# Performance work log

Measured on AMD Instinct MI355X. Metric: run time of the kernel, lower is better.

Reference implementation:

```python
import jax, jax.numpy as jnp
import numpy as np

N_NODES = 100000
N_EDGES = 1000000
D_IN = 256
D_OUT = 64


def setup_inputs() -> dict:
    key = jax.random.key(0)
    k1, k2, k3, k4, k5, k6 = jax.random.split(key, 6)
    x = jax.random.normal(k1, (N_NODES, D_IN), dtype=jnp.float32)
    # Xavier-style uniform init: stdv = 1/sqrt(output_dim)
    stdv = 1.0 / np.sqrt(D_OUT)
    weight = jax.random.uniform(k2, (D_IN, D_OUT), dtype=jnp.float32, minval=-stdv, maxval=stdv)
    adj_vals = jax.random.uniform(k3, (N_EDGES,), dtype=jnp.float32)
    prelu_a = jnp.full((1,), 0.25, dtype=jnp.float32)  # nn.PReLU default
    row = jax.random.randint(k4, (N_EDGES,), 0, N_NODES, dtype=jnp.int32)
    col = jax.random.randint(k5, (N_EDGES,), 0, N_NODES, dtype=jnp.int32)
    return {"x": x, "weight": weight, "adj_vals": adj_vals, "prelu_a": prelu_a,
            "row": row, "col": col}


def reference(x, weight, adj_vals, prelu_a, row, col):
    # dense GEMM: [N, D_in] @ [D_in, D_out]
    hidden = x @ weight  # gc_drop=0 -> identity dropout
    # sparse adj spmm: out[i] = sum_{e: row[e]=i} adj_vals[e] * hidden[col[e]]
    msg = adj_vals[:, None] * hidden[col]  # [E, D_out]
    agg = jax.ops.segment_sum(msg, row, num_segments=N_NODES)  # [N, D_out]
    # PReLU with single shared slope
    out = jnp.where(agg > 0, agg, prelu_a * agg)
    return out
```

## Files before the change

### kernel.cpp

```cpp
#include <hip/hip_runtime.h>

#define N_NODES 100000
#define N_EDGES 1000000
#define D_IN    256
#define D_OUT   64

#define BKT_SHIFT   8
#define NODES_PER_B 256
#define N_BKT       391
#define BKT_CAP     3072
#define EPB         8192
#define BIN_BLOCKS  123
#define GEMM_BLOCKS 782
#define NUM_TILES   6250

typedef __attribute__((ext_vector_type(8))) short short8;
typedef __attribute__((ext_vector_type(4))) float f32x4;

__device__ __forceinline__ unsigned short f2bf(float f) {
    unsigned int u = __float_as_uint(f);
    u = (u + 0x7fffu + ((u >> 16) & 1u)) >> 16;
    return (unsigned short)u;
}

__device__ __forceinline__ void mfma_store_tile(
    const short8 afrag[8], const unsigned short wT[64][272],
    unsigned short* __restrict__ hiddenBf, int r0, int n16, int quad)
{
    f32x4 acc[4] = {{0.f,0.f,0.f,0.f},{0.f,0.f,0.f,0.f},
                    {0.f,0.f,0.f,0.f},{0.f,0.f,0.f,0.f}};
#pragma unroll
    for (int ct = 0; ct < 4; ++ct) {
#pragma unroll
        for (int kk = 0; kk < 8; ++kk) {
            short8 b = *(const short8*)&wT[ct * 16 + n16][kk * 32 + quad * 8];
            acc[ct] = __builtin_amdgcn_mfma_f32_16x16x32_bf16(
                afrag[kk], b, acc[ct], 0, 0, 0);
        }
    }
#pragma unroll
    for (int ct = 0; ct < 4; ++ct)
#pragma unroll
        for (int reg = 0; reg < 4; ++reg)
            hiddenBf[(size_t)(r0 + quad * 4 + reg) * D_OUT + ct * 16 + n16]
                = f2bf(acc[ct][reg]);
}

__global__ __launch_bounds__(256, 2) void gemm_bin_kernel(
    const float* __restrict__ x, const float* __restrict__ w,
    unsigned short* __restrict__ hiddenBf,
    const int* __restrict__ row, const int* __restrict__ col,
    const float* __restrict__ adj, int* __restrict__ gCursor,
    int2* __restrict__ edges)
{
    const int t = threadIdx.x;

    if (blockIdx.x < BIN_BLOCKS) {
        __shared__ int cnt[N_BKT];
        __shared__ int cbase[N_BKT];
        __shared__ int cur[N_BKT];

        const int e0 = blockIdx.x * EPB;

        for (int i = t; i < N_BKT; i += 256) cnt[i] = 0;
        __syncthreads();

        for (int i = t; i < EPB; i += 256) {
            int e = e0 + i;
            if (e < N_EDGES) atomicAdd(&cnt[row[e] >> BKT_SHIFT], 1);
        }
        __syncthreads();

        for (int i = t; i < N_BKT; i += 256) {
            int c = cnt[i];
            cbase[i] = c ? atomicAdd(&gCursor[i], c) : 0;
            cur[i] = 0;
        }
        __syncthreads();

        for (int i = t; i < EPB; i += 256) {
            int e = e0 + i;
            if (e < N_EDGES) {
                int r = row[e];
                int b = r >> BKT_SHIFT;
                int off = cbase[b] + atomicAdd(&cur[b], 1);
                if (off < BKT_CAP) {
                    edges[b * BKT_CAP + off] =
                        make_int2(((r & (NODES_PER_B - 1)) << 17) | col[e],
                                  __float_as_int(adj[e]));
                }
            }
        }
        return;
    }

    __shared__ unsigned short wT[64][272];

    for (int i = 0; i < 64; ++i) {
        int idx = t + i * 256;
        int k = idx >> 6, n = idx & 63;
        wT[n][k] = f2bf(w[idx]);
    }
    __syncthreads();

    const int lane = t & 63;
    const int wid  = t >> 6;
    const int n16  = lane & 15;
    const int quad = lane >> 4;

    const int waveGid = (blockIdx.x - BIN_BLOCKS) * 4 + wid;
    const int t0 = waveGid * 2;
    if (t0 >= NUM_TILES) return;

    float4 lo[8], hi[8];
    short8 afrag[8];

    {
        const float* xrow = x + (size_t)(t0 * 16 + n16) * D_IN + quad * 8;
#pragma unroll
        for (int kk = 0; kk < 8; ++kk) {
            lo[kk] = *(const float4*)(xrow + kk * 32);
            hi[kk] = *(const float4*)(xrow + kk * 32 + 4);
        }
    }
#pragma unroll
    for (int kk = 0; kk < 8; ++kk) {
        short8 a;
        a[0] = (short)f2bf(lo[kk].x); a[1] = (short)f2bf(lo[kk].y);
        a[2] = (short)f2bf(lo[kk].z); a[3] = (short)f2bf(lo[kk].w);
        a[4] = (short)f2bf(hi[kk].x); a[5] = (short)f2bf(hi[kk].y);
        a[6] = (short)f2bf(hi[kk].z); a[7] = (short)f2bf(hi[kk].w);
        afrag[kk] = a;
    }

    const int t1 = t0 + 1;
    const bool have1 = t1 < NUM_TILES;
    if (have1) {
        const float* xrow = x + (size_t)(t1 * 16 + n16) * D_IN + quad * 8;
#pragma unroll
        for (int kk = 0; kk < 8; ++kk) {
            lo[kk] = *(const float4*)(xrow + kk * 32);
            hi[kk] = *(const float4*)(xrow + kk * 32 + 4);
        }
    }

    mfma_store_tile(afrag, wT, hiddenBf, t0 * 16, n16, quad);

    if (have1) {
#pragma unroll
        for (int kk = 0; kk < 8; ++kk) {
            short8 a;
            a[0] = (short)f2bf(lo[kk].x); a[1] = (short)f2bf(lo[kk].y);
            a[2] = (short)f2bf(lo[kk].z); a[3] = (short)f2bf(lo[kk].w);
            a[4] = (short)f2bf(hi[kk].x); a[5] = (short)f2bf(hi[kk].y);
            a[6] = (short)f2bf(hi[kk].z); a[7] = (short)f2bf(hi[kk].w);
            afrag[kk] = a;
        }
        mfma_store_tile(afrag, wT, hiddenBf, t1 * 16, n16, quad);
    }
}

__global__ __launch_bounds__(512) void csr_kernel(
    const int2* __restrict__ edges, const int* __restrict__ gCursor,
    int2* __restrict__ csr, unsigned int* __restrict__ startdeg)
{
    __shared__ int cnt[NODES_PER_B];
    __shared__ int cur[NODES_PER_B];

    const int b = blockIdx.x, t = threadIdx.x;
    if (t < NODES_PER_B) cnt[t] = 0;
    __syncthreads();

    const int base = b * BKT_CAP;
    int size = gCursor[b];
    if (size > BKT_CAP) size = BKT_CAP;

    for (int i = t; i < size; i += 512)
        atomicAdd(&cnt[(unsigned)edges[base + i].x >> 17], 1);
    __syncthreads();

    int v = (t < NODES_PER_B) ? cnt[t] : 0;
    for (int off = 1; off < NODES_PER_B; off <<= 1) {
        int tmp = (t < NODES_PER_B && t >= off) ? cnt[t - off] : 0;
        __syncthreads();
        if (t < NODES_PER_B) cnt[t] += tmp;
        __syncthreads();
    }
    if (t < NODES_PER_B) {
        int gstart = base + cnt[t] - v;
        cur[t] = gstart;
        int node = b * NODES_PER_B + t;
        if (node < N_NODES)
            startdeg[node] = ((unsigned)gstart << 11) |
                             (unsigned)(v < 2047 ? v : 2047);
    }
    __syncthreads();

    for (int i = t; i < size; i += 512) {
        int2 rec = edges[base + i];
        int rl = (unsigned)rec.x >> 17;
        int pos = atomicAdd(&cur[rl], 1);
        csr[pos] = make_int2(rec.x & 0x1FFFF, rec.y);
    }
}

__global__ __launch_bounds__(256) void agg_kernel(
    const unsigned short* __restrict__ hiddenBf,
    const unsigned int* __restrict__ startdeg,
    const int2* __restrict__ csr, const float* __restrict__ prelu_a,
    float* __restrict__ out)
{
    const int wid  = threadIdx.x >> 6;
    const int lane = threadIdx.x & 63;
    const int node = blockIdx.x * 4 + wid;

    const unsigned int sd = startdeg[node];
    const int start = sd >> 11;
    const int deg   = sd & 2047;

    float acc = 0.f;
    for (int base = 0; base < deg; base += 64) {
        int take = deg - base;
        if (take > 64) take = 64;
        int2 rec = make_int2(0, 0);
        if (lane < take) rec = csr[start + base + lane];

        int j = 0;
        for (; j + 8 <= take; j += 8) {
            int   c[8]; float v[8]; float h[8];
#pragma unroll
            for (int u = 0; u < 8; ++u) {
                c[u] = __builtin_amdgcn_readlane(rec.x, j + u);
                v[u] = __int_as_float(__builtin_amdgcn_readlane(rec.y, j + u));
            }
#pragma unroll
            for (int u = 0; u < 8; ++u)
                h[u] = __uint_as_float(
                    (unsigned)hiddenBf[(size_t)c[u] * D_OUT + lane] << 16);
#pragma unroll
            for (int u = 0; u < 8; ++u) acc += v[u] * h[u];
        }
        for (; j < take; ++j) {
            int   c = __builtin_amdgcn_readlane(rec.x, j);
            float v = __int_as_float(__builtin_amdgcn_readlane(rec.y, j));
            float h = __uint_as_float(
                (unsigned)hiddenBf[(size_t)c * D_OUT + lane] << 16);
            acc += v * h;
        }
    }
    const float a = prelu_a[0];
    out[(size_t)node * D_OUT + lane] = acc > 0.f ? acc : a * acc;
}

extern "C" void kernel_launch(void* const* d_in, const int* in_sizes, int n_in,
                              void* d_out, int out_size, void* d_ws, size_t ws_size,
                              hipStream_t stream)
{
    const float* x       = (const float*)d_in[0];
    const float* w       = (const float*)d_in[1];
    const float* adj     = (const float*)d_in[2];
    const float* prelu_a = (const float*)d_in[3];
    const int*   row     = (const int*)d_in[4];
    const int*   col     = (const int*)d_in[5];
    float* out = (float*)d_out;

    char* ws = (char*)d_ws;
    unsigned short* hiddenBf = (unsigned short*)(ws);
    int2*  edges    = (int2*)        (ws + 12800000);
    int2*  csr      = (int2*)        (ws + 22409216);
    unsigned int* startdeg = (unsigned int*)(ws + 32018944);
    int*   gCursor  = (int*)         (ws + 32419328);

    hipMemsetAsync(gCursor, 0, N_BKT * sizeof(int), stream);

    gemm_bin_kernel<<<BIN_BLOCKS + GEMM_BLOCKS, 256, 0, stream>>>(
        x, w, hiddenBf, row, col, adj, gCursor, edges);

    csr_kernel<<<N_BKT, 512, 0, stream>>>(edges, gCursor, csr, startdeg);

    agg_kernel<<<N_NODES / 4, 256, 0, stream>>>(hiddenBf, startdeg, csr, prelu_a, out);
}
```

Baseline: 253.8 us.

## Fuse CSR construction and aggregation into one per-bucket kernel with LDS sort

```diff
diff --git a/kernel.cpp b/kernel.cpp
--- a/kernel.cpp
+++ b/kernel.cpp
@@ -22,9 +22,12 @@
     u = (u + 0x7fffu + ((u >> 16) & 1u)) >> 16;
     return (unsigned short)u;
 }
+__device__ __forceinline__ float bf2f(unsigned short h) {
+    return __uint_as_float((unsigned)h << 16);
+}
 
 __device__ __forceinline__ void mfma_store_tile(
-    const short8 afrag[8], const unsigned short wT[64][272],
+    const short8 afrag[8], const unsigned short wT[64][264],
     unsigned short* __restrict__ hiddenBf, int r0, int n16, int quad)
 {
     f32x4 acc[4] = {{0.f,0.f,0.f,0.f},{0.f,0.f,0.f,0.f},
@@ -94,12 +97,18 @@
         return;
     }
 
-    __shared__ unsigned short wT[64][272];
-
-    for (int i = 0; i < 64; ++i) {
-        int idx = t + i * 256;
-        int k = idx >> 6, n = idx & 63;
-        wT[n][k] = f2bf(w[idx]);
+    __shared__ unsigned short wT[64][264];
+
+#pragma unroll
+    for (int i = 0; i < 16; ++i) {
+        int v4 = i * 256 + t;
+        float4 f = ((const float4*)w)[v4];
+        int k = v4 >> 4;
+        int n = (v4 & 15) * 4;
+        wT[n + 0][k] = f2bf(f.x);
+        wT[n + 1][k] = f2bf(f.y);
+        wT[n + 2][k] = f2bf(f.z);
+        wT[n + 3][k] = f2bf(f.w);
     }
     __syncthreads();
 
@@ -160,12 +169,15 @@
     }
 }
 
-__global__ __launch_bounds__(512) void csr_kernel(
+__global__ __launch_bounds__(512) void aggsort_kernel(
+    const unsigned short* __restrict__ hiddenBf,
     const int2* __restrict__ edges, const int* __restrict__ gCursor,
-    int2* __restrict__ csr, unsigned int* __restrict__ startdeg)
-{
-    __shared__ int cnt[NODES_PER_B];
-    __shared__ int cur[NODES_PER_B];
+    const float* __restrict__ prelu_a, float* __restrict__ out)
+{
+    __shared__ int2 srec[BKT_CAP];
+    __shared__ int  cnt[NODES_PER_B];
+    __shared__ int  cur[NODES_PER_B];
+    __shared__ unsigned sdp[NODES_PER_B];
 
     const int b = blockIdx.x, t = threadIdx.x;
     if (t < NODES_PER_B) cnt[t] = 0;
@@ -175,8 +187,13 @@
     int size = gCursor[b];
     if (size > BKT_CAP) size = BKT_CAP;
 
-    for (int i = t; i < size; i += 512)
-        atomicAdd(&cnt[(unsigned)edges[base + i].x >> 17], 1);
+    int2 myrec[6];
+    int nmine = 0;
+    for (int i = t; i < size; i += 512) {
+        int2 rec = edges[base + i];
+        myrec[nmine++] = rec;
+        atomicAdd(&cnt[(unsigned)rec.x >> 17], 1);
+    }
     __syncthreads();
 
     int v = (t < NODES_PER_B) ? cnt[t] : 0;
@@ -187,69 +204,50 @@
         __syncthreads();
     }
     if (t < NODES_PER_B) {
-        int gstart = base + cnt[t] - v;
-        cur[t] = gstart;
-        int node = b * NODES_PER_B + t;
-        if (node < N_NODES)
-            startdeg[node] = ((unsigned)gstart << 11) |
-                             (unsigned)(v < 2047 ? v : 2047);
-    }
-    __syncthreads();
-
-    for (int i = t; i < size; i += 512) {
-        int2 rec = edges[base + i];
-        int rl = (unsigned)rec.x >> 17;
+        int start = cnt[t] - v;
+        cur[t] = start;
+        sdp[t] = ((unsigned)start << 11) | (unsigned)(v < 2047 ? v : 2047);
+    }
+    __syncthreads();
+
+    for (int j = 0; j < nmine; ++j) {
+        int rl  = (unsigned)myrec[j].x >> 17;
         int pos = atomicAdd(&cur[rl], 1);
-        csr[pos] = make_int2(rec.x & 0x1FFFF, rec.y);
-    }
-}
-
-__global__ __launch_bounds__(256) void agg_kernel(
-    const unsigned short* __restrict__ hiddenBf,
-    const unsigned int* __restrict__ startdeg,
-    const int2* __restrict__ csr, const float* __restrict__ prelu_a,
-    float* __restrict__ out)
-{
-    const int wid  = threadIdx.x >> 6;
-    const int lane = threadIdx.x & 63;
-    const int node = blockIdx.x * 4 + wid;
-
-    const unsigned int sd = startdeg[node];
-    const int start = sd >> 11;
-    const int deg   = sd & 2047;
-
-    float acc = 0.f;
-    for (int base = 0; base < deg; base += 64) {
-        int take = deg - base;
-        if (take > 64) take = 64;
-        int2 rec = make_int2(0, 0);
-        if (lane < take) rec = csr[start + base + lane];
-
+        srec[pos] = make_int2(myrec[j].x & 0x1FFFF, myrec[j].y);
+    }
+    __syncthreads();
+
+    const int wave = t >> 6;
+    const int lane = t & 63;
+    const float a = prelu_a[0];
+    const int node0 = b * NODES_PER_B;
+
+    for (int ni = wave; ni < NODES_PER_B; ni += 8) {
+        int node = node0 + ni;
+        if (node >= N_NODES) break;
+        unsigned sd = sdp[ni];
+        int s = sd >> 11;
+        int d = sd & 2047;
+
+        float acc = 0.f;
         int j = 0;
-        for (; j + 8 <= take; j += 8) {
-            int   c[8]; float v[8]; float h[8];
+        for (; j + 8 <= d; j += 8) {
+            float vv[8], hh[8];
 #pragma unroll
             for (int u = 0; u < 8; ++u) {
-                c[u] = __builtin_amdgcn_readlane(rec.x, j + u);
-                v[u] = __int_as_float(__builtin_amdgcn_readlane(rec.y, j + u));
+                int2 r = srec[s + j + u];
+                vv[u] = __int_as_float(r.y);
+                hh[u] = bf2f(hiddenBf[(size_t)r.x * D_OUT + lane]);
             }
 #pragma unroll
-            for (int u = 0; u < 8; ++u)
-                h[u] = __uint_as_float(
-                    (unsigned)hiddenBf[(size_t)c[u] * D_OUT + lane] << 16);
-#pragma unroll
-            for (int u = 0; u < 8; ++u) acc += v[u] * h[u];
-        }
-        for (; j < take; ++j) {
-            int   c = __builtin_amdgcn_readlane(rec.x, j);
-            float v = __int_as_float(__builtin_amdgcn_readlane(rec.y, j));
-            float h = __uint_as_float(
-                (unsigned)hiddenBf[(size_t)c * D_OUT + lane] << 16);
-            acc += v * h;
-        }
-    }
-    const float a = prelu_a[0];
-    out[(size_t)node * D_OUT + lane] = acc > 0.f ? acc : a * acc;
+            for (int u = 0; u < 8; ++u) acc += vv[u] * hh[u];
+        }
+        for (; j < d; ++j) {
+            int2 r = srec[s + j];
+            acc += __int_as_float(r.y) * bf2f(hiddenBf[(size_t)r.x * D_OUT + lane]);
+        }
+        out[(size_t)node * D_OUT + lane] = acc > 0.f ? acc : a * acc;
+    }
 }
 
 extern "C" void kernel_launch(void* const* d_in, const int* in_sizes, int n_in,
@@ -266,17 +264,13 @@
 
     char* ws = (char*)d_ws;
     unsigned short* hiddenBf = (unsigned short*)(ws);
-    int2*  edges    = (int2*)        (ws + 12800000);
-    int2*  csr      = (int2*)        (ws + 22409216);
-    unsigned int* startdeg = (unsigned int*)(ws + 32018944);
-    int*   gCursor  = (int*)         (ws + 32419328);
+    int2* edges   = (int2*)(ws + 12800000);
+    int*  gCursor = (int*) (ws + 22409216);
 
     hipMemsetAsync(gCursor, 0, N_BKT * sizeof(int), stream);
 
     gemm_bin_kernel<<<BIN_BLOCKS + GEMM_BLOCKS, 256, 0, stream>>>(
         x, w, hiddenBf, row, col, adj, gCursor, edges);
 
-    csr_kernel<<<N_BKT, 512, 0, stream>>>(edges, gCursor, csr, startdeg);
-
-    agg_kernel<<<N_NODES / 4, 256, 0, stream>>>(hiddenBf, startdeg, csr, prelu_a, out);
-}
+    aggsort_kernel<<<N_BKT, 512, 0, stream>>>(hiddenBf, edges, gCursor, prelu_a, out);
+}
```

Result: slower. 273.9 us (+7.9%).
